# Optimization experiments

Measured on AMD Instinct MI355X. Metric: run time of the kernel, lower is better.

## Reference

```python
import jax, jax.numpy as jnp
import numpy as np

N = 100_000   # nodes
E = 1_600_000 # edges
G = 64        # graphs in batch
IN_FEAT, H = 8, 16
NUM_CLASSES = 4


def _glorot(key, fi, fo):
    lim = float(np.sqrt(6.0 / (fi + fo)))
    return jax.random.uniform(key, (fi, fo), jnp.float32, -lim, lim)


def setup_inputs() -> dict:
    key = jax.random.key(0)
    ks = jax.random.split(key, 12)
    inp = {
        "x": jax.random.normal(ks[0], (N, IN_FEAT), jnp.float32),
        "edge_src": jax.random.randint(ks[1], (E,), 0, N, dtype=jnp.int32),
        "edge_dst": jax.random.randint(ks[2], (E,), 0, N, dtype=jnp.int32),
        "batch": jnp.sort(jax.random.randint(ks[3], (N,), 0, G, dtype=jnp.int32)),
    }
    dims = [(IN_FEAT, H), (H, 2 * H), (2 * H, 4 * H), (4 * H, 8 * H)]
    for i, (fi, fo) in enumerate(dims, 1):
        inp[f"W{i}"] = _glorot(ks[3 + i], fi, fo)
        inp[f"b{i}"] = jnp.zeros((fo,), jnp.float32)
    # PReLU slopes (torch default init 0.25, single parameter)
    inp["a1"] = jnp.float32(0.25)
    inp["a2"] = jnp.float32(0.25)
    inp["a3"] = jnp.float32(0.25)
    inp["Wlin"] = _glorot(ks[8], 8 * H, NUM_CLASSES)
    inp["blin"] = jnp.zeros((NUM_CLASSES,), jnp.float32)
    return inp


def _prelu(x, a):
    return jnp.where(x >= 0, x, a * x)


def reference(x, edge_src, edge_dst, batch,
              W1, b1, W2, b2, W3, b3, W4, b4,
              a1, a2, a3, Wlin, blin):
    # GCNConv: add self-loops, symmetric normalization D^-1/2 A_hat D^-1/2
    loops = jnp.arange(N, dtype=edge_src.dtype)
    src = jnp.concatenate([edge_src, loops])  # [E+N]
    dst = jnp.concatenate([edge_dst, loops])
    deg = jax.ops.segment_sum(jnp.ones_like(src, jnp.float32), dst, num_segments=N)
    dinv = jax.lax.rsqrt(jnp.maximum(deg, 1.0))
    norm = dinv[src] * dinv[dst]  # [E+N]

    def gcn(h, W, b):
        h = h @ W                                   # [N, Fout]
        msg = h[src] * norm[:, None]                # gather + edge scale
        return jax.ops.segment_sum(msg, dst, num_segments=N) + b

    h = _prelu(gcn(x, W1, b1), a1)
    h = _prelu(gcn(h, W2, b2), a2)
    h = _prelu(gcn(h, W3, b3), a3)
    h = gcn(h, W4, b4)

    # global mean pool over graphs
    sums = jax.ops.segment_sum(h, batch, num_segments=G)          # [G, 8H]
    cnts = jax.ops.segment_sum(jnp.ones((N,), jnp.float32), batch, num_segments=G)
    pooled = sums / jnp.maximum(cnts, 1.0)[:, None]
    # dropout(p=0.25) is identity at inference
    return pooled @ Wlin + blin                                    # [G, 4]
```

## Files before the change

kernel.cpp:

```cpp
#include <hip/hip_runtime.h>
#include <hip/hip_fp16.h>

#define NN 100000
#define NE 1600000
#define NG 64

#define BSHIFT 7
#define BUCKW (1 << BSHIFT)
#define NBUCK ((NN + BUCKW - 1) >> BSHIFT)
#define BIN_CHUNK 8192

union H8 { float4 f4; __half2 h2[4]; };
__device__ __forceinline__ void h8_to_f(const H8& h, float* f) {
    float2 a = __half22float2(h.h2[0]);
    float2 b = __half22float2(h.h2[1]);
    float2 c = __half22float2(h.h2[2]);
    float2 d = __half22float2(h.h2[3]);
    f[0]=a.x; f[1]=a.y; f[2]=b.x; f[3]=b.y; f[4]=c.x; f[5]=c.y; f[6]=d.x; f[7]=d.y;
}
__device__ __forceinline__ H8 f_to_h8(const float* f) {
    H8 h;
    h.h2[0] = __floats2half2_rn(f[0], f[1]);
    h.h2[1] = __floats2half2_rn(f[2], f[3]);
    h.h2[2] = __floats2half2_rn(f[4], f[5]);
    h.h2[3] = __floats2half2_rn(f[6], f[7]);
    return h;
}

__global__ __launch_bounds__(256) void bucket_hist_kernel(const int* __restrict__ dst,
                                                          int* __restrict__ bucket_cnt, int E) {
    __shared__ int h[NBUCK];
    for (int i = threadIdx.x; i < NBUCK; i += 256) h[i] = 0;
    __syncthreads();
    int stride = gridDim.x * 256;
    for (int e = blockIdx.x * 256 + threadIdx.x; e < E; e += stride)
        atomicAdd(&h[dst[e] >> BSHIFT], 1);
    __syncthreads();
    for (int i = threadIdx.x; i < NBUCK; i += 256)
        if (h[i]) atomicAdd(&bucket_cnt[i], h[i]);
}

__global__ void bucket_scan_kernel(const int* __restrict__ bcnt, int* __restrict__ boff,
                                   int* __restrict__ bcur) {
    __shared__ int buf[2][1024];
    int t = threadIdx.x;
    int v = (t < NBUCK) ? bcnt[t] : 0;
    buf[0][t] = v;
    __syncthreads();
    int cur = 0;
    for (int off = 1; off < 1024; off <<= 1) {
        int x = buf[cur][t];
        if (t >= off) x += buf[cur][t - off];
        buf[cur ^ 1][t] = x;
        __syncthreads();
        cur ^= 1;
    }
    if (t < NBUCK) {
        int e = buf[cur][t] - v;
        boff[t] = e;
        bcur[t] = e;
    }
}

__global__ __launch_bounds__(256) void bin_kernel(const int* __restrict__ src,
                                                  const int* __restrict__ dst,
                                                  int* __restrict__ bcur,
                                                  unsigned* __restrict__ binned, int E) {
    __shared__ int h[NBUCK];
    __shared__ int cur[NBUCK];
    for (int i = threadIdx.x; i < NBUCK; i += 256) h[i] = 0;
    __syncthreads();
    int base = blockIdx.x * BIN_CHUNK;
    int end = base + BIN_CHUNK; if (end > E) end = E;
    for (int e = base + threadIdx.x; e < end; e += 256)
        atomicAdd(&h[dst[e] >> BSHIFT], 1);
    __syncthreads();
    for (int i = threadIdx.x; i < NBUCK; i += 256) {
        int c = h[i];
        cur[i] = c ? atomicAdd(&bcur[i], c) : 0;
    }
    __syncthreads();
    for (int e = base + threadIdx.x; e < end; e += 256) {
        unsigned s = (unsigned)src[e], d = (unsigned)dst[e];
        int pos = atomicAdd(&cur[d >> BSHIFT], 1);
        binned[pos] = (s << BSHIFT) | (d & (BUCKW - 1));
    }
}

__global__ __launch_bounds__(256) void deg_dinv_kernel(const unsigned* __restrict__ binned,
                                                       const int* __restrict__ bucket_off,
                                                       const int* __restrict__ bucket_cnt,
                                                       int* __restrict__ deg,
                                                       float* __restrict__ dinv, int n) {
    __shared__ int ldeg[BUCKW];
    int b = blockIdx.x;
    for (int i = threadIdx.x; i < BUCKW; i += 256) ldeg[i] = 0;
    __syncthreads();
    int start = bucket_off[b], cnt = bucket_cnt[b];
    for (int k = threadIdx.x; k < cnt; k += 256)
        atomicAdd(&ldeg[binned[start + k] & (BUCKW - 1)], 1);
    __syncthreads();
    int v0 = b << BSHIFT;
    for (int i = threadIdx.x; i < BUCKW; i += 256) {
        int v = v0 + i;
        if (v < n) {
            int dg = ldeg[i];
            deg[v] = dg;
            dinv[v] = rsqrtf((float)dg + 1.0f);
        }
    }
}

__global__ void scan1_kernel(const int* __restrict__ cntin, int* __restrict__ excl,
                             int* __restrict__ bsum, int n) {
    __shared__ int buf[2][1024];
    int t = threadIdx.x;
    int gid = blockIdx.x * 1024 + t;
    int v = (gid < n) ? cntin[gid] : 0;
    buf[0][t] = v;
    __syncthreads();
    int cur = 0;
    for (int off = 1; off < 1024; off <<= 1) {
        int x = buf[cur][t];
        if (t >= off) x += buf[cur][t - off];
        buf[cur ^ 1][t] = x;
        __syncthreads();
        cur ^= 1;
    }
    int incl = buf[cur][t];
    if (gid < n) excl[gid] = incl - v;
    if (t == 1023) bsum[blockIdx.x] = incl;
}

__global__ void scan2_kernel(int* __restrict__ bsum, int nb) {
    __shared__ int buf[2][128];
    int t = threadIdx.x;
    int v = (t < nb) ? bsum[t] : 0;
    buf[0][t] = v;
    __syncthreads();
    int cur = 0;
    for (int off = 1; off < 128; off <<= 1) {
        int x = buf[cur][t];
        if (t >= off) x += buf[cur][t - off];
        buf[cur ^ 1][t] = x;
        __syncthreads();
        cur ^= 1;
    }
    if (t < nb) bsum[t] = buf[cur][t] - v;
}

__global__ void scan3_kernel(int* __restrict__ excl, const int* __restrict__ bsum, int n) {
    int gid = blockIdx.x * blockDim.x + threadIdx.x;
    if (gid < n) excl[gid] += bsum[gid >> 10];
}

__global__ __launch_bounds__(256) void build2_kernel(const unsigned* __restrict__ binned,
                                                     const int* __restrict__ bucket_off,
                                                     const int* __restrict__ bucket_cnt,
                                                     const int* __restrict__ roff,
                                                     int* __restrict__ csr_src, int n) {
    __shared__ int lcur[BUCKW];
    int b = blockIdx.x;
    int v0 = b << BSHIFT;
    for (int i = threadIdx.x; i < BUCKW; i += 256) {
        int v = v0 + i;
        lcur[i] = (v < n) ? roff[v] : 0;
    }
    __syncthreads();
    int start = bucket_off[b], cnt = bucket_cnt[b];
    for (int k = threadIdx.x; k < cnt; k += 256) {
        unsigned e = binned[start + k];
        int pos = atomicAdd(&lcur[e & (BUCKW - 1)], 1);
        csr_src[pos] = (int)(e >> BSHIFT);
    }
}

__global__ void agg8_kernel(const float* __restrict__ x, const int* __restrict__ row_off,
                            const int* __restrict__ deg, const float* __restrict__ dinv,
                            const int* __restrict__ csr_src, float2* __restrict__ out, int n) {
    int idx = blockIdx.x * blockDim.x + threadIdx.x;
    if (idx >= n * 2) return;
    int v = idx >> 1;
    int c = idx & 1;
    const float4* h4 = (const float4*)x;
    float dvv = dinv[v];
    float4 self = h4[(size_t)v * 2 + c];
    float4 acc = make_float4(self.x * dvv, self.y * dvv, self.z * dvv, self.w * dvv);
    int start = row_off[v], cnt = deg[v];
    const int* __restrict__ row = csr_src + start;
    int j = 0;
    for (; j + 4 <= cnt; j += 4) {
        int s0 = row[j], s1 = row[j + 1], s2 = row[j + 2], s3 = row[j + 3];
        float d0 = dinv[s0], d1 = dinv[s1], d2 = dinv[s2], d3 = dinv[s3];
        float4 a0 = h4[(size_t)s0 * 2 + c];
        float4 a1 = h4[(size_t)s1 * 2 + c];
        float4 a2 = h4[(size_t)s2 * 2 + c];
        float4 a3 = h4[(size_t)s3 * 2 + c];
        acc.x += (a0.x * d0 + a1.x * d1) + (a2.x * d2 + a3.x * d3);
        acc.y += (a0.y * d0 + a1.y * d1) + (a2.y * d2 + a3.y * d3);
        acc.z += (a0.z * d0 + a1.z * d1) + (a2.z * d2 + a3.z * d3);
        acc.w += (a0.w * d0 + a1.w * d1) + (a2.w * d2 + a3.w * d3);
    }
    for (; j < cnt; ++j) {
        int s = row[j];
        float ds = dinv[s];
        float4 a = h4[(size_t)s * 2 + c];
        acc.x += a.x * ds; acc.y += a.y * ds; acc.z += a.z * ds; acc.w += a.w * ds;
    }
    union { float2 f2; __half2 h2[2]; } u;
    u.h2[0] = __floats2half2_rn(acc.x * dvv, acc.y * dvv);
    u.h2[1] = __floats2half2_rn(acc.z * dvv, acc.w * dvv);
    out[idx] = u.f2;
}

template<int FIN>
__global__ void agg_h_kernel(const float4* __restrict__ hs, const int* __restrict__ row_off,
                             const int* __restrict__ deg, const float* __restrict__ dinv,
                             const int* __restrict__ csr_src, float4* __restrict__ out, int n) {
    constexpr int G = FIN / 8;
    int idx = blockIdx.x * blockDim.x + threadIdx.x;
    if (idx >= n * G) return;
    int v = idx / G;
    int c = idx % G;
    float a[8];
    { H8 h; h.f4 = hs[(size_t)v * G + c]; h8_to_f(h, a); }
    int start = row_off[v], cnt = deg[v];
    const int* __restrict__ row = csr_src + start;
    int j = 0;
    for (; j + 8 <= cnt; j += 8) {
        H8 hh[8];
#pragma unroll
        for (int q = 0; q < 8; ++q) hh[q].f4 = hs[(size_t)row[j + q] * G + c];
#pragma unroll
        for (int q = 0; q < 8; ++q) {
            float f[8]; h8_to_f(hh[q], f);
#pragma unroll
            for (int k = 0; k < 8; ++k) a[k] += f[k];
        }
    }
    for (; j + 4 <= cnt; j += 4) {
        H8 h0, h1, h2, h3;
        h0.f4 = hs[(size_t)row[j] * G + c];
        h1.f4 = hs[(size_t)row[j + 1] * G + c];
        h2.f4 = hs[(size_t)row[j + 2] * G + c];
        h3.f4 = hs[(size_t)row[j + 3] * G + c];
        float f0[8], f1[8], f2[8], f3[8];
        h8_to_f(h0, f0); h8_to_f(h1, f1); h8_to_f(h2, f2); h8_to_f(h3, f3);
#pragma unroll
        for (int k = 0; k < 8; ++k) a[k] += (f0[k] + f1[k]) + (f2[k] + f3[k]);
    }
    for (; j < cnt; ++j) {
        H8 h; h.f4 = hs[(size_t)row[j] * G + c];
        float f[8]; h8_to_f(h, f);
#pragma unroll
        for (int k = 0; k < 8; ++k) a[k] += f[k];
    }
    float dv = dinv[v];
#pragma unroll
    for (int k = 0; k < 8; ++k) a[k] *= dv;
    H8 o = f_to_h8(a);
    out[(size_t)v * G + c] = o.f4;
}

template<int FIN, int FOUT, bool SCALE>
__global__ __launch_bounds__(256) void matmul_kernel(
    const float4* __restrict__ tin, const float* __restrict__ W,
    const float* __restrict__ bias, const float* __restrict__ slope,
    const float* __restrict__ dinv, float2* __restrict__ hout, int n) {
    constexpr int TPN = FOUT / 4;
    constexpr int NPB = (256 / TPN) * 4;
    __shared__ float4 Wl[FIN * TPN];
    const float4* Wg = (const float4*)W;
    for (int i = threadIdx.x; i < FIN * TPN; i += 256) Wl[i] = Wg[i];
    __syncthreads();
    int t = threadIdx.x;
    int grp = t / TPN;
    int f4 = t % TPN;
    int v0 = blockIdx.x * NPB + grp * 4;
    float s = slope ? *slope : 1.0f;
    float4 bv = ((const float4*)bias)[f4];
    float4 acc[4];
#pragma unroll
    for (int nn = 0; nn < 4; ++nn) acc[nn] = bv;
#pragma unroll
    for (int i = 0; i < FIN; i += 8) {
        float r[4][8];
#pragma unroll
        for (int nn = 0; nn < 4; ++nn) {
            int v = v0 + nn;
            H8 h;
            h.f4 = (v < n) ? tin[(size_t)v * (FIN / 8) + (i >> 3)]
                           : make_float4(0.f, 0.f, 0.f, 0.f);
            h8_to_f(h, r[nn]);
        }
#pragma unroll
        for (int k = 0; k < 8; ++k) {
            float4 wv = Wl[(i + k) * TPN + f4];
#pragma unroll
            for (int nn = 0; nn < 4; ++nn) {
                float rk = r[nn][k];
                acc[nn].x += wv.x * rk;
                acc[nn].y += wv.y * rk;
                acc[nn].z += wv.z * rk;
                acc[nn].w += wv.w * rk;
            }
        }
    }
#pragma unroll
    for (int nn = 0; nn < 4; ++nn) {
        int v = v0 + nn;
        if (v < n) {
            float m = SCALE ? dinv[v] : 1.0f;
            float ox = (fmaxf(acc[nn].x, 0.f) + s * fminf(acc[nn].x, 0.f)) * m;
            float oy = (fmaxf(acc[nn].y, 0.f) + s * fminf(acc[nn].y, 0.f)) * m;
            float oz = (fmaxf(acc[nn].z, 0.f) + s * fminf(acc[nn].z, 0.f)) * m;
            float ow = (fmaxf(acc[nn].w, 0.f) + s * fminf(acc[nn].w, 0.f)) * m;
            union { float2 f2; __half2 h2[2]; } u;
            u.h2[0] = __floats2half2_rn(ox, oy);
            u.h2[1] = __floats2half2_rn(oz, ow);
            hout[(size_t)v * TPN + f4] = u.f2;
        }
    }
}

__global__ __launch_bounds__(256) void makeM_kernel(
    const float* __restrict__ W4, const float* __restrict__ b4,
    const float* __restrict__ Wlin, const float* __restrict__ blin,
    float* __restrict__ M, float* __restrict__ bb) {
    int t = threadIdx.x;
    int k = t >> 2, c = t & 3;
    float m = 0.f;
    for (int j = 0; j < 128; ++j) m += W4[k * 128 + j] * Wlin[j * 4 + c];
    M[k * 4 + c] = m;
    if (t < 4) {
        float v = blin[t];
        for (int j = 0; j < 128; ++j) v += b4[j] * Wlin[j * 4 + t];
        bb[t] = v;
    }
}

__global__ __launch_bounds__(256) void matmul_z_kernel(
    const float4* __restrict__ tin, const float* __restrict__ W,
    const float* __restrict__ bias, const float* __restrict__ slope,
    const float* __restrict__ dinv, const float* __restrict__ M,
    float4* __restrict__ z, int n) {
    constexpr int FIN = 32, FOUT = 64, TPN = FOUT / 4, NPB = 64;
    __shared__ float4 Wl[FIN * TPN];
    __shared__ float4 Ml[FOUT];
    const float4* Wg = (const float4*)W;
    for (int i = threadIdx.x; i < FIN * TPN; i += 256) Wl[i] = Wg[i];
    if (threadIdx.x < FOUT) Ml[threadIdx.x] = ((const float4*)M)[threadIdx.x];
    __syncthreads();
    int t = threadIdx.x;
    int grp = t / TPN;
    int f4 = t % TPN;
    int v0 = blockIdx.x * NPB + grp * 4;
    float s = *slope;
    float4 bv = ((const float4*)bias)[f4];
    float4 acc[4];
#pragma unroll
    for (int nn = 0; nn < 4; ++nn) acc[nn] = bv;
#pragma unroll
    for (int i = 0; i < FIN; i += 8) {
        float r[4][8];
#pragma unroll
        for (int nn = 0; nn < 4; ++nn) {
            int v = v0 + nn;
            H8 h;
            h.f4 = (v < n) ? tin[(size_t)v * (FIN / 8) + (i >> 3)]
                           : make_float4(0.f, 0.f, 0.f, 0.f);
            h8_to_f(h, r[nn]);
        }
#pragma unroll
        for (int k = 0; k < 8; ++k) {
            float4 wv = Wl[(i + k) * TPN + f4];
#pragma unroll
            for (int nn = 0; nn < 4; ++nn) {
                float rk = r[nn][k];
                acc[nn].x += wv.x * rk;
                acc[nn].y += wv.y * rk;
                acc[nn].z += wv.z * rk;
                acc[nn].w += wv.w * rk;
            }
        }
    }
    float4 m0 = Ml[f4 * 4 + 0];
    float4 m1 = Ml[f4 * 4 + 1];
    float4 m2 = Ml[f4 * 4 + 2];
    float4 m3 = Ml[f4 * 4 + 3];
#pragma unroll
    for (int nn = 0; nn < 4; ++nn) {
        int v = v0 + nn;
        float dvm = (v < n) ? dinv[v] : 0.f;
        float ox = (fmaxf(acc[nn].x, 0.f) + s * fminf(acc[nn].x, 0.f)) * dvm;
        float oy = (fmaxf(acc[nn].y, 0.f) + s * fminf(acc[nn].y, 0.f)) * dvm;
        float oz = (fmaxf(acc[nn].z, 0.f) + s * fminf(acc[nn].z, 0.f)) * dvm;
        float ow = (fmaxf(acc[nn].w, 0.f) + s * fminf(acc[nn].w, 0.f)) * dvm;
        float px = ox * m0.x + oy * m1.x + oz * m2.x + ow * m3.x;
        float py = ox * m0.y + oy * m1.y + oz * m2.y + ow * m3.y;
        float pz = ox * m0.z + oy * m1.z + oz * m2.z + ow * m3.z;
        float pw = ox * m0.w + oy * m1.w + oz * m2.w + ow * m3.w;
#pragma unroll
        for (int mask = 8; mask >= 1; mask >>= 1) {
            px += __shfl_xor(px, mask, 16);
            py += __shfl_xor(py, mask, 16);
            pz += __shfl_xor(pz, mask, 16);
            pw += __shfl_xor(pw, mask, 16);
        }
        if (f4 == 0 && v < n) z[v] = make_float4(px, py, pz, pw);
    }
}

__global__ __launch_bounds__(256) void aggpool4_kernel(
    const float4* __restrict__ z, const int* __restrict__ row_off,
    const int* __restrict__ deg, const float* __restrict__ dinv,
    const int* __restrict__ csr_src, const int* __restrict__ batch,
    float* __restrict__ sums, float* __restrict__ cnt, int n) {
    __shared__ float lacc[NG * 4];
    __shared__ float lcnt[NG];
    int tid = threadIdx.x;
    if (tid < NG * 4) lacc[tid] = 0.f;
    if (tid < NG) lcnt[tid] = 0.f;
    __syncthreads();
    int v = blockIdx.x * 256 + tid;
    bool valid = (v < n);
    float cx = 0.f, cy = 0.f, cz = 0.f, cw = 0.f, rc = 0.f;
    int g = -1;
    if (valid) {
        float4 acc = z[v];
        int start = row_off[v], dcnt = deg[v];
        const int* __restrict__ row = csr_src + start;
        int j = 0;
        for (; j + 4 <= dcnt; j += 4) {
            float4 a0 = z[row[j]];
            float4 a1 = z[row[j + 1]];
            float4 a2 = z[row[j + 2]];
            float4 a3 = z[row[j + 3]];
            acc.x += (a0.x + a1.x) + (a2.x + a3.x);
            acc.y += (a0.y + a1.y) + (a2.y + a3.y);
            acc.z += (a0.z + a1.z) + (a2.z + a3.z);
            acc.w += (a0.w + a1.w) + (a2.w + a3.w);
        }
        for (; j < dcnt; ++j) {
            float4 a = z[row[j]];
            acc.x += a.x; acc.y += a.y; acc.z += a.z; acc.w += a.w;
        }
        float dv = dinv[v];
        cx = acc.x * dv; cy = acc.y * dv; cz = acc.z * dv; cw = acc.w * dv;
        rc = 1.f;
        g = batch[v];
    }
    int g0 = __shfl(g, 0, 64);
    if (__all(g == g0 || !valid)) {
#pragma unroll
        for (int mask = 32; mask >= 1; mask >>= 1) {
            cx += __shfl_xor(cx, mask, 64);
            cy += __shfl_xor(cy, mask, 64);
            cz += __shfl_xor(cz, mask, 64);
            cw += __shfl_xor(cw, mask, 64);
            rc += __shfl_xor(rc, mask, 64);
        }
        if ((tid & 63) == 0) {
            float* lp = &lacc[g0 * 4];
            atomicAdd(lp + 0, cx); atomicAdd(lp + 1, cy);
            atomicAdd(lp + 2, cz); atomicAdd(lp + 3, cw);
            atomicAdd(&lcnt[g0], rc);
        }
    } else if (valid) {
        float* lp = &lacc[g * 4];
        atomicAdd(lp + 0, cx); atomicAdd(lp + 1, cy);
        atomicAdd(lp + 2, cz); atomicAdd(lp + 3, cw);
        atomicAdd(&lcnt[g], 1.f);
    }
    __syncthreads();
    if (tid < NG * 4) {
        float val = lacc[tid];
        if (val != 0.f) atomicAdd(&sums[tid], val);
    }
    if (tid < NG) {
        float val = lcnt[tid];
        if (val != 0.f) atomicAdd(&cnt[tid], val);
    }
}

__global__ void head_kernel(const float* __restrict__ sums, const float* __restrict__ cnt,
                            const float* __restrict__ bb, float* __restrict__ out) {
    int t = threadIdx.x;
    int g = t >> 2, c = t & 3;
    out[t] = sums[t] / fmaxf(cnt[g], 1.f) + bb[c];
}

extern "C" void kernel_launch(void* const* d_in, const int* in_sizes, int n_in,
                              void* d_out, int out_size, void* d_ws, size_t ws_size,
                              hipStream_t stream) {
    const float* x    = (const float*)d_in[0];
    const int* esrc   = (const int*)d_in[1];
    const int* edst   = (const int*)d_in[2];
    const int* batch  = (const int*)d_in[3];
    const float* W1 = (const float*)d_in[4],  *b1 = (const float*)d_in[5];
    const float* W2 = (const float*)d_in[6],  *b2 = (const float*)d_in[7];
    const float* W3 = (const float*)d_in[8],  *b3 = (const float*)d_in[9];
    const float* W4 = (const float*)d_in[10], *b4 = (const float*)d_in[11];
    const float* a1 = (const float*)d_in[12];
    const float* a2 = (const float*)d_in[13];
    const float* a3 = (const float*)d_in[14];
    const float* Wlin = (const float*)d_in[15], *blin = (const float*)d_in[16];
    float* out = (float*)d_out;

    const int N = NN, E = NE;
    const int NB = (N + 1023) / 1024;
    const int NBIN = (E + BIN_CHUNK - 1) / BIN_CHUNK;

    char* w = (char*)d_ws;
    size_t off = 0;
    auto alloc = [&](size_t bytes) { size_t r = off; off += (bytes + 255) & ~(size_t)255; return r; };
    size_t o_bcnt = alloc((size_t)NBUCK * 4);
    size_t o_pool = alloc((size_t)NG * 4 * 4);
    size_t o_cnt  = alloc((size_t)NG * 4);
    size_t zero_bytes = off;
    size_t o_deg  = alloc((size_t)N * 4);
    size_t o_dinv = alloc((size_t)N * 4);
    size_t o_roff = alloc((size_t)N * 4);
    size_t o_boff = alloc((size_t)NBUCK * 4);
    size_t o_bcur = alloc((size_t)NBUCK * 4);
    size_t o_bsum = alloc((size_t)128 * 4);
    size_t o_csrc = alloc((size_t)E * 4);
    size_t o_bin  = alloc((size_t)E * 4);
    size_t o_A    = alloc((size_t)N * 32 * 2);
    size_t o_T    = alloc((size_t)N * 32 * 2);
    size_t o_z    = alloc((size_t)N * 4 * 4);
    size_t o_M    = alloc((size_t)64 * 4 * 4);
    size_t o_bb   = alloc((size_t)4 * 4);
    (void)ws_size;
    int*      bcnt   = (int*)(w + o_bcnt);
    float*    pool   = (float*)(w + o_pool);
    float*    cnt    = (float*)(w + o_cnt);
    int*      deg    = (int*)(w + o_deg);
    float*    dinv   = (float*)(w + o_dinv);
    int*      roff   = (int*)(w + o_roff);
    int*      boff   = (int*)(w + o_boff);
    int*      bcur   = (int*)(w + o_bcur);
    int*      bsum   = (int*)(w + o_bsum);
    int*      csrc   = (int*)(w + o_csrc);
    unsigned* binned = (unsigned*)(w + o_bin);
    char*     A      = (char*)(w + o_A);
    char*     T      = (char*)(w + o_T);
    float4*   z      = (float4*)(w + o_z);
    float*    M      = (float*)(w + o_M);
    float*    bb     = (float*)(w + o_bb);

    hipMemsetAsync(w, 0, zero_bytes, stream);

    makeM_kernel<<<1, 256, 0, stream>>>(W4, b4, Wlin, blin, M, bb);

    bucket_hist_kernel<<<256, 256, 0, stream>>>(edst, bcnt, E);
    bucket_scan_kernel<<<1, 1024, 0, stream>>>(bcnt, boff, bcur);
    bin_kernel<<<NBIN, 256, 0, stream>>>(esrc, edst, bcur, binned, E);
    deg_dinv_kernel<<<NBUCK, 256, 0, stream>>>(binned, boff, bcnt, deg, dinv, N);
    scan1_kernel<<<NB, 1024, 0, stream>>>(deg, roff, bsum, N);
    scan2_kernel<<<1, 128, 0, stream>>>(bsum, NB);
    scan3_kernel<<<(N + 255) / 256, 256, 0, stream>>>(roff, bsum, N);
    build2_kernel<<<NBUCK, 256, 0, stream>>>(binned, boff, bcnt, roff, csrc, N);

    agg8_kernel<<<(N * 2 + 255) / 256, 256, 0, stream>>>(x, roff, deg, dinv, csrc, (float2*)T, N);
    matmul_kernel<8, 16, true><<<(N + 255) / 256, 256, 0, stream>>>(
        (const float4*)T, W1, b1, a1, dinv, (float2*)A, N);

    agg_h_kernel<16><<<(N * 2 + 255) / 256, 256, 0, stream>>>(
        (const float4*)A, roff, deg, dinv, csrc, (float4*)T, N);
    matmul_kernel<16, 32, true><<<(N + 127) / 128, 256, 0, stream>>>(
        (const float4*)T, W2, b2, a2, dinv, (float2*)A, N);

    agg_h_kernel<32><<<(N * 4 + 255) / 256, 256, 0, stream>>>(
        (const float4*)A, roff, deg, dinv, csrc, (float4*)T, N);
    matmul_z_kernel<<<(N + 63) / 64, 256, 0, stream>>>(
        (const float4*)T, W3, b3, a3, dinv, M, z, N);

    aggpool4_kernel<<<(N + 255) / 256, 256, 0, stream>>>(
        z, roff, deg, dinv, csrc, batch, pool, cnt, N);
    head_kernel<<<1, 256, 0, stream>>>(pool, cnt, bb, out);
}
```

Measured before the change: 266.3 us.

## Sort nodes by degree to balance aggregation work across warps

Adds a counting sort of nodes by in-degree (histogram, scan, placement) that builds a permutation. The three aggregation kernels then process nodes in that order, so threads in a wavefront have similar neighbor counts and less divergence in the loop lengths. The cost is three extra small launches, an extra perm lookup, and scattered output writes and loss of locality for each node's own row. Degrees are Poisson around 16, so the imbalance being removed is modest.

```diff
diff --git a/kernel.cpp b/kernel.cpp
--- a/kernel.cpp
+++ b/kernel.cpp
@@ -9,6 +9,7 @@
 #define BUCKW (1 << BSHIFT)
 #define NBUCK ((NN + BUCKW - 1) >> BSHIFT)
 #define BIN_CHUNK 8192
+#define NDEGC 64
 
 union H8 { float4 f4; __half2 h2[4]; };
 __device__ __forceinline__ void h8_to_f(const H8& h, float* f) {
@@ -175,12 +176,62 @@
     }
 }
 
+__global__ __launch_bounds__(256) void dhist_kernel(const int* __restrict__ deg,
+                                                    int* __restrict__ dhist, int n) {
+    __shared__ int h[NDEGC];
+    int t = threadIdx.x;
+    if (t < NDEGC) h[t] = 0;
+    __syncthreads();
+    int v = blockIdx.x * 256 + t;
+    if (v < n) atomicAdd(&h[min(deg[v], NDEGC - 1)], 1);
+    __syncthreads();
+    if (t < NDEGC && h[t]) atomicAdd(&dhist[t], h[t]);
+}
+
+__global__ void dscan_kernel(const int* __restrict__ dhist, int* __restrict__ dcur) {
+    __shared__ int buf[2][NDEGC];
+    int t = threadIdx.x;
+    int v = dhist[t];
+    buf[0][t] = v;
+    __syncthreads();
+    int cur = 0;
+    for (int off = 1; off < NDEGC; off <<= 1) {
+        int x = buf[cur][t];
+        if (t >= off) x += buf[cur][t - off];
+        buf[cur ^ 1][t] = x;
+        __syncthreads();
+        cur ^= 1;
+    }
+    dcur[t] = buf[cur][t] - v;
+}
+
+__global__ __launch_bounds__(256) void dplace_kernel(const int* __restrict__ deg,
+                                                     int* __restrict__ dcur,
+                                                     int* __restrict__ perm, int n) {
+    __shared__ int h[NDEGC];
+    __shared__ int cur[NDEGC];
+    int t = threadIdx.x;
+    if (t < NDEGC) h[t] = 0;
+    __syncthreads();
+    int v = blockIdx.x * 256 + t;
+    int dc = -1;
+    if (v < n) { dc = min(deg[v], NDEGC - 1); atomicAdd(&h[dc], 1); }
+    __syncthreads();
+    if (t < NDEGC) { int c = h[t]; cur[t] = c ? atomicAdd(&dcur[t], c) : 0; }
+    __syncthreads();
+    if (v < n) {
+        int pos = atomicAdd(&cur[dc], 1);
+        perm[pos] = v;
+    }
+}
+
 __global__ void agg8_kernel(const float* __restrict__ x, const int* __restrict__ row_off,
                             const int* __restrict__ deg, const float* __restrict__ dinv,
-                            const int* __restrict__ csr_src, float2* __restrict__ out, int n) {
+                            const int* __restrict__ csr_src, const int* __restrict__ perm,
+                            float2* __restrict__ out, int n) {
     int idx = blockIdx.x * blockDim.x + threadIdx.x;
     if (idx >= n * 2) return;
-    int v = idx >> 1;
+    int v = perm[idx >> 1];
     int c = idx & 1;
     const float4* h4 = (const float4*)x;
     float dvv = dinv[v];
@@ -210,17 +261,18 @@
     union { float2 f2; __half2 h2[2]; } u;
     u.h2[0] = __floats2half2_rn(acc.x * dvv, acc.y * dvv);
     u.h2[1] = __floats2half2_rn(acc.z * dvv, acc.w * dvv);
-    out[idx] = u.f2;
+    out[(size_t)v * 2 + c] = u.f2;
 }
 
 template<int FIN>
 __global__ void agg_h_kernel(const float4* __restrict__ hs, const int* __restrict__ row_off,
                              const int* __restrict__ deg, const float* __restrict__ dinv,
-                             const int* __restrict__ csr_src, float4* __restrict__ out, int n) {
+                             const int* __restrict__ csr_src, const int* __restrict__ perm,
+                             float4* __restrict__ out, int n) {
     constexpr int G = FIN / 8;
     int idx = blockIdx.x * blockDim.x + threadIdx.x;
     if (idx >= n * G) return;
-    int v = idx / G;
+    int v = perm[idx / G];
     int c = idx % G;
     float a[8];
     { H8 h; h.f4 = hs[(size_t)v * G + c]; h8_to_f(h, a); }
@@ -510,20 +562,24 @@
     const int N = NN, E = NE;
     const int NB = (N + 1023) / 1024;
     const int NBIN = (E + BIN_CHUNK - 1) / BIN_CHUNK;
+    const int NBLK = (N + 255) / 256;
 
     char* w = (char*)d_ws;
     size_t off = 0;
     auto alloc = [&](size_t bytes) { size_t r = off; off += (bytes + 255) & ~(size_t)255; return r; };
-    size_t o_bcnt = alloc((size_t)NBUCK * 4);
-    size_t o_pool = alloc((size_t)NG * 4 * 4);
-    size_t o_cnt  = alloc((size_t)NG * 4);
+    size_t o_bcnt  = alloc((size_t)NBUCK * 4);
+    size_t o_pool  = alloc((size_t)NG * 4 * 4);
+    size_t o_cnt   = alloc((size_t)NG * 4);
+    size_t o_dhist = alloc((size_t)NDEGC * 4);
     size_t zero_bytes = off;
     size_t o_deg  = alloc((size_t)N * 4);
     size_t o_dinv = alloc((size_t)N * 4);
     size_t o_roff = alloc((size_t)N * 4);
+    size_t o_perm = alloc((size_t)N * 4);
     size_t o_boff = alloc((size_t)NBUCK * 4);
     size_t o_bcur = alloc((size_t)NBUCK * 4);
     size_t o_bsum = alloc((size_t)128 * 4);
+    size_t o_dcur = alloc((size_t)NDEGC * 4);
     size_t o_csrc = alloc((size_t)E * 4);
     size_t o_bin  = alloc((size_t)E * 4);
     size_t o_A    = alloc((size_t)N * 32 * 2);
@@ -535,12 +591,15 @@
     int*      bcnt   = (int*)(w + o_bcnt);
     float*    pool   = (float*)(w + o_pool);
     float*    cnt    = (float*)(w + o_cnt);
+    int*      dhist  = (int*)(w + o_dhist);
     int*      deg    = (int*)(w + o_deg);
     float*    dinv   = (float*)(w + o_dinv);
     int*      roff   = (int*)(w + o_roff);
+    int*      perm   = (int*)(w + o_perm);
     int*      boff   = (int*)(w + o_boff);
     int*      bcur   = (int*)(w + o_bcur);
     int*      bsum   = (int*)(w + o_bsum);
+    int*      dcur   = (int*)(w + o_dcur);
     int*      csrc   = (int*)(w + o_csrc);
     unsigned* binned = (unsigned*)(w + o_bin);
     char*     A      = (char*)(w + o_A);
@@ -562,17 +621,22 @@
     scan3_kernel<<<(N + 255) / 256, 256, 0, stream>>>(roff, bsum, N);
     build2_kernel<<<NBUCK, 256, 0, stream>>>(binned, boff, bcnt, roff, csrc, N);
 
-    agg8_kernel<<<(N * 2 + 255) / 256, 256, 0, stream>>>(x, roff, deg, dinv, csrc, (float2*)T, N);
+    dhist_kernel<<<NBLK, 256, 0, stream>>>(deg, dhist, N);
+    dscan_kernel<<<1, NDEGC, 0, stream>>>(dhist, dcur);
+    dplace_kernel<<<NBLK, 256, 0, stream>>>(deg, dcur, perm, N);
+
+    agg8_kernel<<<(N * 2 + 255) / 256, 256, 0, stream>>>(x, roff, deg, dinv, csrc, perm,
+                                                         (float2*)T, N);
     matmul_kernel<8, 16, true><<<(N + 255) / 256, 256, 0, stream>>>(
         (const float4*)T, W1, b1, a1, dinv, (float2*)A, N);
 
     agg_h_kernel<16><<<(N * 2 + 255) / 256, 256, 0, stream>>>(
-        (const float4*)A, roff, deg, dinv, csrc, (float4*)T, N);
+        (const float4*)A, roff, deg, dinv, csrc, perm, (float4*)T, N);
     matmul_kernel<16, 32, true><<<(N + 127) / 128, 256, 0, stream>>>(
         (const float4*)T, W2, b2, a2, dinv, (float2*)A, N);
 
     agg_h_kernel<32><<<(N * 4 + 255) / 256, 256, 0, stream>>>(
-        (const float4*)A, roff, deg, dinv, csrc, (float4*)T, N);
+        (const float4*)A, roff, deg, dinv, csrc, perm, (float4*)T, N);
     matmul_z_kernel<<<(N + 63) / 64, 256, 0, stream>>>(
         (const float4*)T, W3, b3, a3, dinv, M, z, N);
 
```

Result: slower. 301.4 us (+13.2%).

## Fuse per-layer aggregation with the dense transform, PReLU and dinv scaling

Applied to the files above, without the earlier changes.

Each GCN layer's gather-aggregate kernel now also performs the following weight multiply, bias, PReLU and dinv scaling. Lanes that share a node exchange their partial feature vectors with wave shuffles, and the weights are held in shared memory. This removes three separate matmul kernel launches and the round trip of the intermediate aggregated tensor through global memory. The cost is more registers and FMA work per thread inside the latency-bound gather kernels, which may lower occupancy, and the 4-then-8 unrolled tail in the layer-2/3 aggregation is dropped.

```diff
diff --git a/kernel.cpp b/kernel.cpp
--- a/kernel.cpp
+++ b/kernel.cpp
@@ -25,6 +25,9 @@
     h.h2[2] = __floats2half2_rn(f[4], f[5]);
     h.h2[3] = __floats2half2_rn(f[6], f[7]);
     return h;
+}
+__device__ __forceinline__ float prelu_f(float x, float s) {
+    return fmaxf(x, 0.f) + s * fminf(x, 0.f);
 }
 
 __global__ __launch_bounds__(256) void bucket_hist_kernel(const int* __restrict__ dst,
@@ -175,10 +178,32 @@
     }
 }
 
-__global__ void agg8_kernel(const float* __restrict__ x, const int* __restrict__ row_off,
-                            const int* __restrict__ deg, const float* __restrict__ dinv,
-                            const int* __restrict__ csr_src, float2* __restrict__ out, int n) {
-    int idx = blockIdx.x * blockDim.x + threadIdx.x;
+__global__ __launch_bounds__(256) void makeM_kernel(
+    const float* __restrict__ W4, const float* __restrict__ b4,
+    const float* __restrict__ Wlin, const float* __restrict__ blin,
+    float* __restrict__ M, float* __restrict__ bb) {
+    int t = threadIdx.x;
+    int k = t >> 2, c = t & 3;
+    float m = 0.f;
+    for (int j = 0; j < 128; ++j) m += W4[k * 128 + j] * Wlin[j * 4 + c];
+    M[k * 4 + c] = m;
+    if (t < 4) {
+        float v = blin[t];
+        for (int j = 0; j < 128; ++j) v += b4[j] * Wlin[j * 4 + t];
+        bb[t] = v;
+    }
+}
+
+__global__ __launch_bounds__(256) void aggmm1_kernel(
+    const float* __restrict__ x, const int* __restrict__ row_off,
+    const int* __restrict__ deg, const float* __restrict__ dinv,
+    const int* __restrict__ csr_src, const float* __restrict__ W1,
+    const float* __restrict__ b1, const float* __restrict__ a1,
+    float4* __restrict__ Aout, int n) {
+    __shared__ float Wl[8 * 16];
+    for (int i = threadIdx.x; i < 8 * 16; i += 256) Wl[i] = W1[i];
+    __syncthreads();
+    int idx = blockIdx.x * 256 + threadIdx.x;
     if (idx >= n * 2) return;
     int v = idx >> 1;
     int c = idx & 1;
@@ -193,13 +218,13 @@
         int s0 = row[j], s1 = row[j + 1], s2 = row[j + 2], s3 = row[j + 3];
         float d0 = dinv[s0], d1 = dinv[s1], d2 = dinv[s2], d3 = dinv[s3];
         float4 a0 = h4[(size_t)s0 * 2 + c];
-        float4 a1 = h4[(size_t)s1 * 2 + c];
+        float4 a1v = h4[(size_t)s1 * 2 + c];
         float4 a2 = h4[(size_t)s2 * 2 + c];
         float4 a3 = h4[(size_t)s3 * 2 + c];
-        acc.x += (a0.x * d0 + a1.x * d1) + (a2.x * d2 + a3.x * d3);
-        acc.y += (a0.y * d0 + a1.y * d1) + (a2.y * d2 + a3.y * d3);
-        acc.z += (a0.z * d0 + a1.z * d1) + (a2.z * d2 + a3.z * d3);
-        acc.w += (a0.w * d0 + a1.w * d1) + (a2.w * d2 + a3.w * d3);
+        acc.x += (a0.x * d0 + a1v.x * d1) + (a2.x * d2 + a3.x * d3);
+        acc.y += (a0.y * d0 + a1v.y * d1) + (a2.y * d2 + a3.y * d3);
+        acc.z += (a0.z * d0 + a1v.z * d1) + (a2.z * d2 + a3.z * d3);
+        acc.w += (a0.w * d0 + a1v.w * d1) + (a2.w * d2 + a3.w * d3);
     }
     for (; j < cnt; ++j) {
         int s = row[j];
@@ -207,30 +232,53 @@
         float4 a = h4[(size_t)s * 2 + c];
         acc.x += a.x * ds; acc.y += a.y * ds; acc.z += a.z * ds; acc.w += a.w * ds;
     }
-    union { float2 f2; __half2 h2[2]; } u;
-    u.h2[0] = __floats2half2_rn(acc.x * dvv, acc.y * dvv);
-    u.h2[1] = __floats2half2_rn(acc.z * dvv, acc.w * dvv);
-    out[idx] = u.f2;
-}
-
-template<int FIN>
-__global__ void agg_h_kernel(const float4* __restrict__ hs, const int* __restrict__ row_off,
-                             const int* __restrict__ deg, const float* __restrict__ dinv,
-                             const int* __restrict__ csr_src, float4* __restrict__ out, int n) {
-    constexpr int G = FIN / 8;
-    int idx = blockIdx.x * blockDim.x + threadIdx.x;
-    if (idx >= n * G) return;
-    int v = idx / G;
-    int c = idx % G;
+    float t[4] = { acc.x * dvv, acc.y * dvv, acc.z * dvv, acc.w * dvv };
+    float po[4];
+#pragma unroll
+    for (int k = 0; k < 4; ++k) po[k] = __shfl_xor(t[k], 1, 64);
+    int ob = c * 8;
+    int e0 = c * 4, e1 = 4 - e0;
+    float accm[8];
+#pragma unroll
+    for (int q = 0; q < 8; ++q) accm[q] = b1[ob + q];
+#pragma unroll
+    for (int k = 0; k < 4; ++k) {
+        float r1 = t[k], r2 = po[k];
+        const float* w1 = &Wl[(e0 + k) * 16 + ob];
+        const float* w2 = &Wl[(e1 + k) * 16 + ob];
+#pragma unroll
+        for (int q = 0; q < 8; ++q) accm[q] += r1 * w1[q] + r2 * w2[q];
+    }
+    float s = *a1;
+    float o[8];
+#pragma unroll
+    for (int q = 0; q < 8; ++q) o[q] = prelu_f(accm[q], s) * dvv;
+    H8 h = f_to_h8(o);
+    Aout[(size_t)v * 2 + c] = h.f4;
+}
+
+__global__ __launch_bounds__(256) void aggmm2_kernel(
+    const float4* __restrict__ hs, const int* __restrict__ row_off,
+    const int* __restrict__ deg, const float* __restrict__ dinv,
+    const int* __restrict__ csr_src, const float* __restrict__ W2,
+    const float* __restrict__ b2, const float* __restrict__ a2,
+    float4* __restrict__ Aout, int n) {
+    __shared__ float Wl[16 * 32];
+    for (int i = threadIdx.x; i < 16 * 32; i += 256) Wl[i] = W2[i];
+    __syncthreads();
+    int idx = blockIdx.x * 256 + threadIdx.x;
+    if (idx >= n * 2) return;
+    int v = idx >> 1;
+    int c = idx & 1;
     float a[8];
-    { H8 h; h.f4 = hs[(size_t)v * G + c]; h8_to_f(h, a); }
+    { H8 h; h.f4 = hs[(size_t)v * 2 + c]; h8_to_f(h, a); }
     int start = row_off[v], cnt = deg[v];
     const int* __restrict__ row = csr_src + start;
     int j = 0;
     for (; j + 8 <= cnt; j += 8) {
         H8 hh[8];
 #pragma unroll
-        for (int q = 0; q < 8; ++q) hh[q].f4 = hs[(size_t)row[j + q] * G + c];
+        for (int q = 0; q < 8; ++q) hh[q].f4 = hs[(size_t)row[j + q] * 2 + c];
 #pragma unroll
         for (int q = 0; q < 8; ++q) {
             float f[8]; h8_to_f(hh[q], f);
@@ -238,177 +286,121 @@
             for (int k = 0; k < 8; ++k) a[k] += f[k];
         }
     }
-    for (; j + 4 <= cnt; j += 4) {
-        H8 h0, h1, h2, h3;
-        h0.f4 = hs[(size_t)row[j] * G + c];
-        h1.f4 = hs[(size_t)row[j + 1] * G + c];
-        h2.f4 = hs[(size_t)row[j + 2] * G + c];
-        h3.f4 = hs[(size_t)row[j + 3] * G + c];
-        float f0[8], f1[8], f2[8], f3[8];
-        h8_to_f(h0, f0); h8_to_f(h1, f1); h8_to_f(h2, f2); h8_to_f(h3, f3);
-#pragma unroll
-        for (int k = 0; k < 8; ++k) a[k] += (f0[k] + f1[k]) + (f2[k] + f3[k]);
-    }
     for (; j < cnt; ++j) {
-        H8 h; h.f4 = hs[(size_t)row[j] * G + c];
+        H8 h; h.f4 = hs[(size_t)row[j] * 2 + c];
         float f[8]; h8_to_f(h, f);
 #pragma unroll
         for (int k = 0; k < 8; ++k) a[k] += f[k];
     }
-    float dv = dinv[v];
-#pragma unroll
-    for (int k = 0; k < 8; ++k) a[k] *= dv;
-    H8 o = f_to_h8(a);
-    out[(size_t)v * G + c] = o.f4;
-}
-
-template<int FIN, int FOUT, bool SCALE>
-__global__ __launch_bounds__(256) void matmul_kernel(
-    const float4* __restrict__ tin, const float* __restrict__ W,
-    const float* __restrict__ bias, const float* __restrict__ slope,
-    const float* __restrict__ dinv, float2* __restrict__ hout, int n) {
-    constexpr int TPN = FOUT / 4;
-    constexpr int NPB = (256 / TPN) * 4;
-    __shared__ float4 Wl[FIN * TPN];
-    const float4* Wg = (const float4*)W;
-    for (int i = threadIdx.x; i < FIN * TPN; i += 256) Wl[i] = Wg[i];
-    __syncthreads();
-    int t = threadIdx.x;
-    int grp = t / TPN;
-    int f4 = t % TPN;
-    int v0 = blockIdx.x * NPB + grp * 4;
-    float s = slope ? *slope : 1.0f;
-    float4 bv = ((const float4*)bias)[f4];
-    float4 acc[4];
-#pragma unroll
-    for (int nn = 0; nn < 4; ++nn) acc[nn] = bv;
-#pragma unroll
-    for (int i = 0; i < FIN; i += 8) {
-        float r[4][8];
-#pragma unroll
-        for (int nn = 0; nn < 4; ++nn) {
-            int v = v0 + nn;
-            H8 h;
-            h.f4 = (v < n) ? tin[(size_t)v * (FIN / 8) + (i >> 3)]
-                           : make_float4(0.f, 0.f, 0.f, 0.f);
-            h8_to_f(h, r[nn]);
-        }
+    float dvv = dinv[v];
+#pragma unroll
+    for (int k = 0; k < 8; ++k) a[k] *= dvv;
+    float pa[8];
+#pragma unroll
+    for (int k = 0; k < 8; ++k) pa[k] = __shfl_xor(a[k], 1, 64);
+    int ob = c * 16;
+    int e0 = c * 8, e1 = 8 - e0;
+    float accm[16];
+#pragma unroll
+    for (int q = 0; q < 16; ++q) accm[q] = b2[ob + q];
+#pragma unroll
+    for (int k = 0; k < 8; ++k) {
+        float r1 = a[k], r2 = pa[k];
+        const float* w1 = &Wl[(e0 + k) * 32 + ob];
+        const float* w2 = &Wl[(e1 + k) * 32 + ob];
+#pragma unroll
+        for (int q = 0; q < 16; ++q) accm[q] += r1 * w1[q] + r2 * w2[q];
+    }
+    float s = *a2;
+    float o[16];
+#pragma unroll
+    for (int q = 0; q < 16; ++q) o[q] = prelu_f(accm[q], s) * dvv;
+    H8 h0 = f_to_h8(o);
+    H8 h1 = f_to_h8(o + 8);
+    Aout[(size_t)v * 4 + c * 2 + 0] = h0.f4;
+    Aout[(size_t)v * 4 + c * 2 + 1] = h1.f4;
+}
+
+__global__ __launch_bounds__(256) void aggmm3_kernel(
+    const float4* __restrict__ hs, const int* __restrict__ row_off,
+    const int* __restrict__ deg, const float* __restrict__ dinv,
+    const int* __restrict__ csr_src, const float* __restrict__ W3,
+    const float* __restrict__ b3, const float* __restrict__ a3,
+    const float* __restrict__ M, float4* __restrict__ z, int n) {
+    __shared__ float Wl[32 * 64];
+    __shared__ float Ml[64 * 4];
+    for (int i = threadIdx.x; i < 32 * 64; i += 256) Wl[i] = W3[i];
+    if (threadIdx.x < 64 * 4 && threadIdx.x < 256) {  }
+    for (int i = threadIdx.x; i < 64 * 4; i += 256) Ml[i] = M[i];
+    __syncthreads();
+    int idx = blockIdx.x * 256 + threadIdx.x;
+    if (idx >= n * 4) return;
+    int v = idx >> 2;
+    int c = idx & 3;
+    float a[8];
+    { H8 h; h.f4 = hs[(size_t)v * 4 + c]; h8_to_f(h, a); }
+    int start = row_off[v], cnt = deg[v];
+    const int* __restrict__ row = csr_src + start;
+    int j = 0;
+    for (; j + 8 <= cnt; j += 8) {
+        H8 hh[8];
+#pragma unroll
+        for (int q = 0; q < 8; ++q) hh[q].f4 = hs[(size_t)row[j + q] * 4 + c];
+#pragma unroll
+        for (int q = 0; q < 8; ++q) {
+            float f[8]; h8_to_f(hh[q], f);
+#pragma unroll
+            for (int k = 0; k < 8; ++k) a[k] += f[k];
+        }
+    }
+    for (; j < cnt; ++j) {
+        H8 h; h.f4 = hs[(size_t)row[j] * 4 + c];
+        float f[8]; h8_to_f(h, f);
+#pragma unroll
+        for (int k = 0; k < 8; ++k) a[k] += f[k];
+    }
+    float dvv = dinv[v];
+#pragma unroll
+    for (int k = 0; k < 8; ++k) a[k] *= dvv;
+    int ob = c * 16;
+    float accm[16];
+#pragma unroll
+    for (int q = 0; q < 16; ++q) accm[q] = b3[ob + q];
+#pragma unroll
+    for (int m = 0; m < 4; ++m) {
+        float cur[8];
+        if (m == 0) {
+#pragma unroll
+            for (int k = 0; k < 8; ++k) cur[k] = a[k];
+        } else {
+#pragma unroll
+            for (int k = 0; k < 8; ++k) cur[k] = __shfl_xor(a[k], m, 64);
+        }
+        int eb = (c ^ m) * 8;
 #pragma unroll
         for (int k = 0; k < 8; ++k) {
-            float4 wv = Wl[(i + k) * TPN + f4];
-#pragma unroll
-            for (int nn = 0; nn < 4; ++nn) {
-                float rk = r[nn][k];
-                acc[nn].x += wv.x * rk;
-                acc[nn].y += wv.y * rk;
-                acc[nn].z += wv.z * rk;
-                acc[nn].w += wv.w * rk;
-            }
-        }
-    }
-#pragma unroll
-    for (int nn = 0; nn < 4; ++nn) {
-        int v = v0 + nn;
-        if (v < n) {
-            float m = SCALE ? dinv[v] : 1.0f;
-            float ox = (fmaxf(acc[nn].x, 0.f) + s * fminf(acc[nn].x, 0.f)) * m;
-            float oy = (fmaxf(acc[nn].y, 0.f) + s * fminf(acc[nn].y, 0.f)) * m;
-            float oz = (fmaxf(acc[nn].z, 0.f) + s * fminf(acc[nn].z, 0.f)) * m;
-            float ow = (fmaxf(acc[nn].w, 0.f) + s * fminf(acc[nn].w, 0.f)) * m;
-            union { float2 f2; __half2 h2[2]; } u;
-            u.h2[0] = __floats2half2_rn(ox, oy);
-            u.h2[1] = __floats2half2_rn(oz, ow);
-            hout[(size_t)v * TPN + f4] = u.f2;
-        }
-    }
-}
-
-__global__ __launch_bounds__(256) void makeM_kernel(
-    const float* __restrict__ W4, const float* __restrict__ b4,
-    const float* __restrict__ Wlin, const float* __restrict__ blin,
-    float* __restrict__ M, float* __restrict__ bb) {
-    int t = threadIdx.x;
-    int k = t >> 2, c = t & 3;
-    float m = 0.f;
-    for (int j = 0; j < 128; ++j) m += W4[k * 128 + j] * Wlin[j * 4 + c];
-    M[k * 4 + c] = m;
-    if (t < 4) {
-        float v = blin[t];
-        for (int j = 0; j < 128; ++j) v += b4[j] * Wlin[j * 4 + t];
-        bb[t] = v;
-    }
-}
-
-__global__ __launch_bounds__(256) void matmul_z_kernel(
-    const float4* __restrict__ tin, const float* __restrict__ W,
-    const float* __restrict__ bias, const float* __restrict__ slope,
-    const float* __restrict__ dinv, const float* __restrict__ M,
-    float4* __restrict__ z, int n) {
-    constexpr int FIN = 32, FOUT = 64, TPN = FOUT / 4, NPB = 64;
-    __shared__ float4 Wl[FIN * TPN];
-    __shared__ float4 Ml[FOUT];
-    const float4* Wg = (const float4*)W;
-    for (int i = threadIdx.x; i < FIN * TPN; i += 256) Wl[i] = Wg[i];
-    if (threadIdx.x < FOUT) Ml[threadIdx.x] = ((const float4*)M)[threadIdx.x];
-    __syncthreads();
-    int t = threadIdx.x;
-    int grp = t / TPN;
-    int f4 = t % TPN;
-    int v0 = blockIdx.x * NPB + grp * 4;
-    float s = *slope;
-    float4 bv = ((const float4*)bias)[f4];
-    float4 acc[4];
-#pragma unroll
-    for (int nn = 0; nn < 4; ++nn) acc[nn] = bv;
-#pragma unroll
-    for (int i = 0; i < FIN; i += 8) {
-        float r[4][8];
-#pragma unroll
-        for (int nn = 0; nn < 4; ++nn) {
-            int v = v0 + nn;
-            H8 h;
-            h.f4 = (v < n) ? tin[(size_t)v * (FIN / 8) + (i >> 3)]
-                           : make_float4(0.f, 0.f, 0.f, 0.f);
-            h8_to_f(h, r[nn]);
-        }
-#pragma unroll
-        for (int k = 0; k < 8; ++k) {
-            float4 wv = Wl[(i + k) * TPN + f4];
-#pragma unroll
-            for (int nn = 0; nn < 4; ++nn) {
-                float rk = r[nn][k];
-                acc[nn].x += wv.x * rk;
-                acc[nn].y += wv.y * rk;
-                acc[nn].z += wv.z * rk;
-                acc[nn].w += wv.w * rk;
-            }
-        }
-    }
-    float4 m0 = Ml[f4 * 4 + 0];
-    float4 m1 = Ml[f4 * 4 + 1];
-    float4 m2 = Ml[f4 * 4 + 2];
-    float4 m3 = Ml[f4 * 4 + 3];
-#pragma unroll
-    for (int nn = 0; nn < 4; ++nn) {
-        int v = v0 + nn;
-        float dvm = (v < n) ? dinv[v] : 0.f;
-        float ox = (fmaxf(acc[nn].x, 0.f) + s * fminf(acc[nn].x, 0.f)) * dvm;
-        float oy = (fmaxf(acc[nn].y, 0.f) + s * fminf(acc[nn].y, 0.f)) * dvm;
-        float oz = (fmaxf(acc[nn].z, 0.f) + s * fminf(acc[nn].z, 0.f)) * dvm;
-        float ow = (fmaxf(acc[nn].w, 0.f) + s * fminf(acc[nn].w, 0.f)) * dvm;
-        float px = ox * m0.x + oy * m1.x + oz * m2.x + ow * m3.x;
-        float py = ox * m0.y + oy * m1.y + oz * m2.y + ow * m3.y;
-        float pz = ox * m0.z + oy * m1.z + oz * m2.z + ow * m3.z;
-        float pw = ox * m0.w + oy * m1.w + oz * m2.w + ow * m3.w;
-#pragma unroll
-        for (int mask = 8; mask >= 1; mask >>= 1) {
-            px += __shfl_xor(px, mask, 16);
-            py += __shfl_xor(py, mask, 16);
-            pz += __shfl_xor(pz, mask, 16);
-            pw += __shfl_xor(pw, mask, 16);
-        }
-        if (f4 == 0 && v < n) z[v] = make_float4(px, py, pz, pw);
-    }
+            float rk = cur[k];
+            const float* wp = &Wl[(eb + k) * 64 + ob];
+#pragma unroll
+            for (int q = 0; q < 16; ++q) accm[q] += rk * wp[q];
+        }
+    }
+    float s = *a3;
+    float px = 0.f, py = 0.f, pz = 0.f, pw = 0.f;
+#pragma unroll
+    for (int q = 0; q < 16; ++q) {
+        float o = prelu_f(accm[q], s) * dvv;
+        const float* mp = &Ml[(ob + q) * 4];
+        px += o * mp[0]; py += o * mp[1]; pz += o * mp[2]; pw += o * mp[3];
+    }
+#pragma unroll
+    for (int mask = 1; mask <= 2; mask <<= 1) {
+        px += __shfl_xor(px, mask, 64);
+        py += __shfl_xor(py, mask, 64);
+        pz += __shfl_xor(pz, mask, 64);
+        pw += __shfl_xor(pw, mask, 64);
+    }
+    if (c == 0) z[v] = make_float4(px, py, pz, pw);
 }
 
 __global__ __launch_bounds__(256) void aggpool4_kernel(
@@ -526,8 +518,8 @@
     size_t o_bsum = alloc((size_t)128 * 4);
     size_t o_csrc = alloc((size_t)E * 4);
     size_t o_bin  = alloc((size_t)E * 4);
-    size_t o_A    = alloc((size_t)N * 32 * 2);
-    size_t o_T    = alloc((size_t)N * 32 * 2);
+    size_t o_A1   = alloc((size_t)N * 16 * 2);
+    size_t o_A2   = alloc((size_t)N * 32 * 2);
     size_t o_z    = alloc((size_t)N * 4 * 4);
     size_t o_M    = alloc((size_t)64 * 4 * 4);
     size_t o_bb   = alloc((size_t)4 * 4);
@@ -543,8 +535,8 @@
     int*      bsum   = (int*)(w + o_bsum);
     int*      csrc   = (int*)(w + o_csrc);
     unsigned* binned = (unsigned*)(w + o_bin);
-    char*     A      = (char*)(w + o_A);
-    char*     T      = (char*)(w + o_T);
+    float4*   A1     = (float4*)(w + o_A1);
+    float4*   A2     = (float4*)(w + o_A2);
     float4*   z      = (float4*)(w + o_z);
     float*    M      = (float*)(w + o_M);
     float*    bb     = (float*)(w + o_bb);
@@ -562,19 +554,14 @@
     scan3_kernel<<<(N + 255) / 256, 256, 0, stream>>>(roff, bsum, N);
     build2_kernel<<<NBUCK, 256, 0, stream>>>(binned, boff, bcnt, roff, csrc, N);
 
-    agg8_kernel<<<(N * 2 + 255) / 256, 256, 0, stream>>>(x, roff, deg, dinv, csrc, (float2*)T, N);
-    matmul_kernel<8, 16, true><<<(N + 255) / 256, 256, 0, stream>>>(
-        (const float4*)T, W1, b1, a1, dinv, (float2*)A, N);
-
-    agg_h_kernel<16><<<(N * 2 + 255) / 256, 256, 0, stream>>>(
-        (const float4*)A, roff, deg, dinv, csrc, (float4*)T, N);
-    matmul_kernel<16, 32, true><<<(N + 127) / 128, 256, 0, stream>>>(
-        (const float4*)T, W2, b2, a2, dinv, (float2*)A, N);
-
-    agg_h_kernel<32><<<(N * 4 + 255) / 256, 256, 0, stream>>>(
-        (const float4*)A, roff, deg, dinv, csrc, (float4*)T, N);
-    matmul_z_kernel<<<(N + 63) / 64, 256, 0, stream>>>(
-        (const float4*)T, W3, b3, a3, dinv, M, z, N);
+    aggmm1_kernel<<<(N * 2 + 255) / 256, 256, 0, stream>>>(
+        x, roff, deg, dinv, csrc, W1, b1, a1, A1, N);
+
+    aggmm2_kernel<<<(N * 2 + 255) / 256, 256, 0, stream>>>(
+        A1, roff, deg, dinv, csrc, W2, b2, a2, A2, N);
+
+    aggmm3_kernel<<<(N * 4 + 255) / 256, 256, 0, stream>>>(
+        A2, roff, deg, dinv, csrc, W3, b3, a3, M, z, N);
 
     aggpool4_kernel<<<(N + 255) / 256, 256, 0, stream>>>(
         z, roff, deg, dinv, csrc, batch, pool, cnt, N);
```

Result: faster. 258.3 us (-3.0%).
